# Performance work log

Hardware: AMD Instinct MI355X
Metric: run time of the kernel (lower is better)

## Reference

```python
import jax, jax.numpy as jnp
import numpy as np

B, N, M, D, NHEAD, FF, C, K = 2, 16384, 2048, 256, 8, 512, 50, 3
HID = 128          # embed/pos hidden
HEAD_HID = 256     # seg head hidden
L = 4              # depth
EPS = 1e-5


def setup_inputs() -> dict:
    key = jax.random.key(0)
    ks = jax.random.split(key, 32)
    g = lambda i, shape: jax.random.normal(ks[i], shape, dtype=jnp.float32) * 0.02
    z = lambda shape: jnp.zeros(shape, jnp.float32)
    o = lambda shape: jnp.ones(shape, jnp.float32)
    return {
        "xyz": jax.random.normal(ks[0], (B, N, 3), dtype=jnp.float32),
        "embed_w1": g(1, (3, HID)), "embed_b1": z((HID,)),
        "embed_w2": g(2, (HID, D)), "embed_b2": z((D,)),
        "pos_w1": g(3, (3, HID)), "pos_b1": z((HID,)),
        "pos_w2": g(4, (HID, D)), "pos_b2": z((D,)),
        "Wq": g(5, (L, D, D)), "bq": z((L, D)),
        "Wk": g(6, (L, D, D)), "bk": z((L, D)),
        "Wv": g(7, (L, D, D)), "bv": z((L, D)),
        "Wo": g(8, (L, D, D)), "bo": z((L, D)),
        "ln1_s": o((L, D)), "ln1_b": z((L, D)),
        "W1": g(9, (L, D, FF)), "b1": z((L, FF)),
        "W2": g(10, (L, FF, D)), "b2": z((L, D)),
        "ln2_s": o((L, D)), "ln2_b": z((L, D)),
        "head_w1": g(11, (D, HEAD_HID)), "head_b1": z((HEAD_HID,)),
        "head_w2": g(12, (HEAD_HID, C)), "head_b2": z((C,)),
    }


def _ln(x, s, b):
    m = x.mean(-1, keepdims=True)
    v = ((x - m) ** 2).mean(-1, keepdims=True)
    return (x - m) / jnp.sqrt(v + EPS) * s + b


def reference(xyz, embed_w1, embed_b1, embed_w2, embed_b2,
              pos_w1, pos_b1, pos_w2, pos_b2,
              Wq, bq, Wk, bk, Wv, bv, Wo, bo, ln1_s, ln1_b,
              W1, b1, W2, b2, ln2_s, ln2_b,
              head_w1, head_b1, head_w2, head_b2):
    # deterministic token subsample (replaces randperm stub): strided pick of M points
    stride = N // M
    tok = xyz[:, ::stride, :][:, :M]                                  # [B,M,3]
    # per-point embed + learned positional encoding
    x = jax.nn.relu(tok @ embed_w1 + embed_b1) @ embed_w2 + embed_b2  # [B,M,D]
    x = x + jax.nn.relu(tok @ pos_w1 + pos_b1) @ pos_w2 + pos_b2
    dh = D // NHEAD
    scale = 1.0 / jnp.sqrt(jnp.float32(dh))

    def layer(x, p):
        wq, bq_, wk, bk_, wv, bv_, wo, bo_, l1s, l1b, w1, b1_, w2, b2_, l2s, l2b = p
        # pre-norm MHSA
        y = _ln(x, l1s, l1b)
        q = (y @ wq + bq_).reshape(B, M, NHEAD, dh)
        k = (y @ wk + bk_).reshape(B, M, NHEAD, dh)
        v = (y @ wv + bv_).reshape(B, M, NHEAD, dh)
        att = jax.nn.softmax(jnp.einsum('bqhd,bkhd->bhqk', q, k) * scale, axis=-1)
        o = jnp.einsum('bhqk,bkhd->bqhd', att, v).reshape(B, M, D)
        x = x + o @ wo + bo_
        # pre-norm FFN (gelu, exact erf as in torch)
        y = _ln(x, l2s, l2b)
        x = x + jax.nn.gelu(y @ w1 + b1_, approximate=False) @ w2 + b2_
        return x, None

    x, _ = jax.lax.scan(layer, x, (Wq, bq, Wk, bk, Wv, bv, Wo, bo,
                                   ln1_s, ln1_b, W1, b1, W2, b2, ln2_s, ln2_b))
    logits_tok = jax.nn.relu(x @ head_w1 + head_b1) @ head_w2 + head_b2  # [B,M,C]

    # kNN propagation N->M: dist^2 = |q|^2 + |k|^2 - 2 q.k, topk smallest
    q2 = (xyz ** 2).sum(-1)[..., None]            # [B,N,1]
    k2 = (tok ** 2).sum(-1)[:, None, :]           # [B,1,M]
    dist = q2 + k2 - 2.0 * jnp.einsum('bnd,bmd->bnm', xyz, tok)
    dist = jax.lax.stop_gradient(jnp.maximum(dist, 0.0))
    idx = jax.lax.top_k(-dist, K)[1]              # [B,N,K]
    logits_nk = logits_tok[jnp.arange(B)[:, None, None], idx]  # [B,N,K,C]
    return logits_nk.mean(axis=2)                 # [B,N,C]
```

## Files before the change

kernel.cpp:

```cpp
#include <hip/hip_runtime.h>
#include <hip/hip_bf16.h>
#include <math.h>

#define B_ 2
#define N_ 16384
#define M_ 2048
#define D_ 256
#define NHEAD_ 8
#define DH_ 32
#define FF_ 512
#define C_ 50
#define HID_ 128
#define HHID_ 256
#define L_ 4
#define EPS_ 1e-5f
#define TOK_ (B_*M_)
#define QSCALE_ 0.25507604155757994f

typedef short short8 __attribute__((ext_vector_type(8)));
typedef short short4_t __attribute__((ext_vector_type(4)));
typedef float f32x4 __attribute__((ext_vector_type(4)));

__device__ __forceinline__ short f2bf(float f) {
  union { float f; unsigned u; } c; c.f = f;
  unsigned u = c.u;
  unsigned r = (u + 0x7FFFu + ((u >> 16) & 1u)) >> 16;
  return (short)r;
}
__device__ __forceinline__ float fast_exp2(float x) {
  float r;
  asm("v_exp_f32 %0, %1" : "=v"(r) : "v"(x));
  return r;
}
__device__ __forceinline__ unsigned cvt_pk_bf16(float lo, float hi) {
  unsigned r;
  asm("v_cvt_pk_bf16_f32 %0, %1, %2" : "=v"(r) : "v"(lo), "v"(hi));
  return r;
}

__device__ __forceinline__ void stage16(const short* __restrict__ g, short* lds,
                                        int rowStride, int tid) {
  int row = tid >> 2, gr = tid & 3;
  int kg = gr ^ (row & 3);
  __builtin_amdgcn_global_load_lds(
      (const __attribute__((address_space(1))) void*)(g + (size_t)row * rowStride + kg * 8),
      (__attribute__((address_space(3))) void*)(lds + tid * 8),
      16, 0, 0);
}

__global__ __launch_bounds__(256) void wconv_all(
    const float* __restrict__ Wq, const float* __restrict__ Wk,
    const float* __restrict__ Wv, const float* __restrict__ Wo,
    const float* __restrict__ W1, const float* __restrict__ W2,
    const float* __restrict__ h1,
    short* __restrict__ WqT, short* __restrict__ WkT,
    short* __restrict__ WvT, short* __restrict__ WoT,
    short* __restrict__ W1T, short* __restrict__ W2T, short* __restrict__ h1T) {
  int bid = blockIdx.x;
  const float* W; short* WT; int Kd, Nd, tn, tk;
  if (bid < 256) {
    int mat = bid >> 6, rem = bid & 63, l = rem >> 4, t = rem & 15;
    W  = (mat == 0 ? Wq : mat == 1 ? Wk : mat == 2 ? Wv : Wo) + l * 65536;
    WT = (mat == 0 ? WqT : mat == 1 ? WkT : mat == 2 ? WvT : WoT) + l * 65536;
    Kd = 256; Nd = 256; tn = t & 3; tk = t >> 2;
  } else if (bid < 384) {
    int rem = bid - 256, l = rem >> 5, t = rem & 31;
    W = W1 + l * 131072; WT = W1T + l * 131072;
    Kd = 256; Nd = 512; tn = t & 7; tk = t >> 3;
  } else if (bid < 512) {
    int rem = bid - 384, l = rem >> 5, t = rem & 31;
    W = W2 + l * 131072; WT = W2T + l * 131072;
    Kd = 512; Nd = 256; tn = t & 3; tk = t >> 2;
  } else {
    int t = bid - 512;
    W = h1; WT = h1T; Kd = 256; Nd = 256; tn = t & 3; tk = t >> 2;
  }
  int n0 = tn * 64, k0 = tk * 64;
  __shared__ short ts[64][72];
  int tid = threadIdx.x;
  #pragma unroll
  for (int i = 0; i < 4; ++i) {
    int r = i * 16 + (tid >> 4);
    int c4 = (tid & 15) * 4;
    float4 v = *(const float4*)&W[(size_t)(k0 + r) * Nd + n0 + c4];
    ts[c4 + 0][r] = f2bf(v.x);
    ts[c4 + 1][r] = f2bf(v.y);
    ts[c4 + 2][r] = f2bf(v.z);
    ts[c4 + 3][r] = f2bf(v.w);
  }
  __syncthreads();
  #pragma unroll
  for (int i = 0; i < 2; ++i) {
    int n = i * 32 + (tid >> 3);
    int kc = (tid & 7) * 8;
    *(short8*)&WT[(size_t)(n0 + n) * Kd + k0 + kc] = *(short8*)&ts[n][kc];
  }
}

__global__ __launch_bounds__(128) void embed_kernel(
    const float* __restrict__ xyz,
    const float* __restrict__ ew1, const float* __restrict__ eb1,
    const float* __restrict__ ew2, const float* __restrict__ eb2,
    const float* __restrict__ pw1, const float* __restrict__ pb1,
    const float* __restrict__ pw2, const float* __restrict__ pb2,
    float* __restrict__ x) {
  int t = blockIdx.x;
  int b = t / M_, m = t % M_;
  const float* p = xyz + ((size_t)b * N_ + (size_t)m * 8) * 3;
  float t0 = p[0], t1 = p[1], t2 = p[2];
  __shared__ float he[HID_], hp[HID_];
  int j = threadIdx.x;
  {
    float a = fmaf(t0, ew1[j], fmaf(t1, ew1[HID_ + j], fmaf(t2, ew1[2 * HID_ + j], eb1[j])));
    he[j] = fmaxf(a, 0.f);
    float c = fmaf(t0, pw1[j], fmaf(t1, pw1[HID_ + j], fmaf(t2, pw1[2 * HID_ + j], pb1[j])));
    hp[j] = fmaxf(c, 0.f);
  }
  __syncthreads();
  for (int d = j; d < D_; d += HID_) {
    float acc = eb2[d] + pb2[d];
    for (int k = 0; k < HID_; ++k) {
      acc = fmaf(he[k], ew2[k * D_ + d], acc);
      acc = fmaf(hp[k], pw2[k * D_ + d], acc);
    }
    x[(size_t)t * D_ + d] = acc;
  }
}

__global__ __launch_bounds__(256) void ln_fused(
    const float* __restrict__ x, const float* __restrict__ pa,
    const float* __restrict__ pb, const float* __restrict__ bias,
    const float* __restrict__ s, const float* __restrict__ bb,
    float* __restrict__ xw, short* __restrict__ y16) {
  int r = blockIdx.x * 4 + (threadIdx.x >> 6);
  int t = threadIdx.x & 63;
  float4 v = ((const float4*)(x + (size_t)r * D_))[t];
  if (pa) {
    float4 a = ((const float4*)(pa + (size_t)r * D_))[t];
    float4 c = ((const float4*)(pb + (size_t)r * D_))[t];
    float4 bi = ((const float4*)bias)[t];
    v.x += a.x + c.x + bi.x;
    v.y += a.y + c.y + bi.y;
    v.z += a.z + c.z + bi.z;
    v.w += a.w + c.w + bi.w;
    ((float4*)(xw + (size_t)r * D_))[t] = v;
  }
  float sum = v.x + v.y + v.z + v.w;
  #pragma unroll
  for (int o = 1; o < 64; o <<= 1) sum += __shfl_xor(sum, o, 64);
  float mean = sum * (1.f / D_);
  float dx = v.x - mean, dy = v.y - mean, dz = v.z - mean, dw = v.w - mean;
  float vs = dx * dx + dy * dy + dz * dz + dw * dw;
  #pragma unroll
  for (int o = 1; o < 64; o <<= 1) vs += __shfl_xor(vs, o, 64);
  float inv = 1.0f / sqrtf(vs * (1.f / D_) + EPS_);
  float4 sv = ((const float4*)s)[t];
  float4 bv = ((const float4*)bb)[t];
  short4_t ov;
  ov[0] = f2bf(dx * inv * sv.x + bv.x);
  ov[1] = f2bf(dy * inv * sv.y + bv.y);
  ov[2] = f2bf(dz * inv * sv.z + bv.z);
  ov[3] = f2bf(dw * inv * sv.w + bv.w);
  *(short4_t*)(y16 + (size_t)r * D_ + t * 4) = ov;
}

__global__ __launch_bounds__(256) void head2_kernel(
    const float* __restrict__ pa, const float* __restrict__ pb,
    const float* __restrict__ b1h, const float* __restrict__ w2,
    const float* __restrict__ b2, float* __restrict__ lt) {
  __shared__ float ys[4][HHID_];
  int w = threadIdx.x >> 6, l = threadIdx.x & 63;
  int t = blockIdx.x * 4 + w;
  float4 a = ((const float4*)(pa + (size_t)t * HHID_))[l];
  float4 c = ((const float4*)(pb + (size_t)t * HHID_))[l];
  float4 bi = ((const float4*)b1h)[l];
  float4 v;
  v.x = fmaxf(a.x + c.x + bi.x, 0.f);
  v.y = fmaxf(a.y + c.y + bi.y, 0.f);
  v.z = fmaxf(a.z + c.z + bi.z, 0.f);
  v.w = fmaxf(a.w + c.w + bi.w, 0.f);
  *(float4*)&ys[w][l * 4] = v;
  int cc = l < C_ ? l : 0;
  float a0 = 0.f, a1 = 0.f, a2 = 0.f, a3 = 0.f;
  #pragma unroll 4
  for (int k = 0; k < HHID_; k += 4) {
    a0 = fmaf(ys[w][k + 0], w2[(k + 0) * C_ + cc], a0);
    a1 = fmaf(ys[w][k + 1], w2[(k + 1) * C_ + cc], a1);
    a2 = fmaf(ys[w][k + 2], w2[(k + 2) * C_ + cc], a2);
    a3 = fmaf(ys[w][k + 3], w2[(k + 3) * C_ + cc], a3);
  }
  if (l < C_) lt[(size_t)t * C_ + l] = (a0 + a1) + (a2 + a3) + b2[l];
}

template <int ACT, int RES>
__device__ __forceinline__ void gemm16_body(
    const short* __restrict__ A16, const short* __restrict__ WT,
    const float* __restrict__ bias, const float* __restrict__ R,
    float* __restrict__ C, short* __restrict__ C16, short* __restrict__ VT,
    float oscale, int K, int Ncols, int m0, int n0) {
  __shared__ short As[64][32];
  __shared__ short Bs[64][32];
  int tid = threadIdx.x;
  int w = tid >> 6, l = tid & 63;
  int lq = l & 15, lg = l >> 4;
  int wr = (w & 1) * 32, wc = (w >> 1) * 32;
  int ga = (lg ^ (lq & 3)) * 8;
  f32x4 acc00 = {0.f, 0.f, 0.f, 0.f};
  f32x4 acc01 = {0.f, 0.f, 0.f, 0.f};
  f32x4 acc10 = {0.f, 0.f, 0.f, 0.f};
  f32x4 acc11 = {0.f, 0.f, 0.f, 0.f};
  for (int kk = 0; kk < K; kk += 32) {
    __syncthreads();
    stage16(A16 + (size_t)m0 * K + kk, &As[0][0], K, tid);
    stage16(WT + (size_t)n0 * K + kk, &Bs[0][0], K, tid);
    __syncthreads();
    short8 a0 = *(short8*)&As[wr + lq][ga];
    short8 a1 = *(short8*)&As[wr + 16 + lq][ga];
    short8 b0 = *(short8*)&Bs[wc + lq][ga];
    short8 b1 = *(short8*)&Bs[wc + 16 + lq][ga];
    acc00 = __builtin_amdgcn_mfma_f32_16x16x32_bf16(a0, b0, acc00, 0, 0, 0);
    acc01 = __builtin_amdgcn_mfma_f32_16x16x32_bf16(a0, b1, acc01, 0, 0, 0);
    acc10 = __builtin_amdgcn_mfma_f32_16x16x32_bf16(a1, b0, acc10, 0, 0, 0);
    acc11 = __builtin_amdgcn_mfma_f32_16x16x32_bf16(a1, b1, acc11, 0, 0, 0);
  }
  #pragma unroll
  for (int fi = 0; fi < 2; ++fi) {
    int row = m0 + wr + fi * 16 + lg * 4;
    #pragma unroll
    for (int fj = 0; fj < 2; ++fj) {
      int col = n0 + wc + fj * 16 + lq;
      short4_t vt4;
      #pragma unroll
      for (int r = 0; r < 4; ++r) {
        float v = (fi == 0 ? (fj == 0 ? acc00[r] : acc01[r])
                           : (fj == 0 ? acc10[r] : acc11[r])) + bias[col];
        if (ACT == 1) v = fmaxf(v, 0.f);
        else if (ACT == 2) v = 0.5f * v * (1.f + erff(v * 0.70710678118654752f));
        if (RES) v += R[(size_t)(row + r) * Ncols + col];
        if (C)   C[(size_t)(row + r) * Ncols + col] = v;
        if (C16) C16[(size_t)(row + r) * Ncols + col] = f2bf(v * oscale);
        if (VT)  vt4[r] = f2bf(v);
      }
      if (VT) {
        int bb = row >> 11, mm = row & (M_ - 1);
        *(short4_t*)&VT[((size_t)(bb * 256 + col)) * M_ + mm] = vt4;
      }
    }
  }
}

template <int ACT, int RES>
__global__ __launch_bounds__(256) void gemm16(
    const short* __restrict__ A16, const short* __restrict__ WT,
    const float* __restrict__ bias, const float* __restrict__ R,
    float* __restrict__ C, short* __restrict__ C16,
    int K, int Ncols) {
  gemm16_body<ACT, RES>(A16, WT, bias, R, C, C16, nullptr, 1.f, K, Ncols,
                        blockIdx.y * 64, blockIdx.x * 64);
}

__global__ __launch_bounds__(256) void gemm16_part(
    const short* __restrict__ A16, const short* __restrict__ WT,
    float* __restrict__ P, int K, int Klen, int Ncols) {
  __shared__ short As[64][32];
  __shared__ short Bs[64][32];
  int tid = threadIdx.x;
  int w = tid >> 6, l = tid & 63;
  int lq = l & 15, lg = l >> 4;
  int wr = (w & 1) * 32, wc = (w >> 1) * 32;
  int ga = (lg ^ (lq & 3)) * 8;
  int m0 = blockIdx.y * 64, n0 = blockIdx.x * 64;
  int k0 = blockIdx.z * Klen;
  f32x4 acc00 = {0.f, 0.f, 0.f, 0.f};
  f32x4 acc01 = {0.f, 0.f, 0.f, 0.f};
  f32x4 acc10 = {0.f, 0.f, 0.f, 0.f};
  f32x4 acc11 = {0.f, 0.f, 0.f, 0.f};
  for (int kk = k0; kk < k0 + Klen; kk += 32) {
    __syncthreads();
    stage16(A16 + (size_t)m0 * K + kk, &As[0][0], K, tid);
    stage16(WT + (size_t)n0 * K + kk, &Bs[0][0], K, tid);
    __syncthreads();
    short8 a0 = *(short8*)&As[wr + lq][ga];
    short8 a1 = *(short8*)&As[wr + 16 + lq][ga];
    short8 b0 = *(short8*)&Bs[wc + lq][ga];
    short8 b1 = *(short8*)&Bs[wc + 16 + lq][ga];
    acc00 = __builtin_amdgcn_mfma_f32_16x16x32_bf16(a0, b0, acc00, 0, 0, 0);
    acc01 = __builtin_amdgcn_mfma_f32_16x16x32_bf16(a0, b1, acc01, 0, 0, 0);
    acc10 = __builtin_amdgcn_mfma_f32_16x16x32_bf16(a1, b0, acc10, 0, 0, 0);
    acc11 = __builtin_amdgcn_mfma_f32_16x16x32_bf16(a1, b1, acc11, 0, 0, 0);
  }
  float* Pp = P + (size_t)blockIdx.z * TOK_ * Ncols;
  #pragma unroll
  for (int fi = 0; fi < 2; ++fi) {
    int row = m0 + wr + fi * 16 + lg * 4;
    #pragma unroll
    for (int fj = 0; fj < 2; ++fj) {
      int col = n0 + wc + fj * 16 + lq;
      #pragma unroll
      for (int r = 0; r < 4; ++r) {
        float v = (fi == 0 ? (fj == 0 ? acc00[r] : acc01[r])
                           : (fj == 0 ? acc10[r] : acc11[r]));
        Pp[(size_t)(row + r) * Ncols + col] = v;
      }
    }
  }
}

__global__ __launch_bounds__(256) void qkv16(
    const short* __restrict__ A16,
    const short* __restrict__ WqT, const short* __restrict__ WkT, const short* __restrict__ WvT,
    const float* __restrict__ bq, const float* __restrict__ bk, const float* __restrict__ bv,
    short* __restrict__ q16, short* __restrict__ k16, short* __restrict__ vt16) {
  int sel = blockIdx.x >> 2;
  int n0 = (blockIdx.x & 3) << 6;
  int m0 = blockIdx.y * 64;
  if (sel == 0) {
    gemm16_body<0, 0>(A16, WqT, bq, nullptr, nullptr, q16, nullptr, QSCALE_, D_, D_, m0, n0);
  } else if (sel == 1) {
    gemm16_body<0, 0>(A16, WkT, bk, nullptr, nullptr, k16, nullptr, 1.f, D_, D_, m0, n0);
  } else {
    gemm16_body<0, 0>(A16, WvT, bv, nullptr, nullptr, nullptr, vt16, 1.f, D_, D_, m0, n0);
  }
}

__global__ __launch_bounds__(256) void wo_split(
    const float* __restrict__ po0, const float* __restrict__ po1,
    const float* __restrict__ pl, const short* __restrict__ WT,
    float* __restrict__ P) {
  __shared__ short As[64][136];
  __shared__ short Bs[64][32];
  int tid = threadIdx.x;
  int w = tid >> 6, l = tid & 63;
  int m0 = blockIdx.y * 64, n0 = blockIdx.x * 64;
  int half = blockIdx.z;
  int c2 = l * 2;
  int hh = half * 4 + (c2 >> 5);
  int d0 = c2 & 31;
  #pragma unroll 4
  for (int c = 0; c < 16; ++c) {
    int t = w * 16 + c;
    int row = m0 + t;
    int bb = row >> 11, mm = row & (M_ - 1);
    size_t f = (size_t)(bb * NHEAD_ + hh) * M_ + mm;
    float inv = 1.f / (pl[f] + pl[16 * M_ + f]);
    float v0 = (po0[f * 32 + d0] + po1[f * 32 + d0]) * inv;
    float v1 = (po0[f * 32 + d0 + 1] + po1[f * 32 + d0 + 1]) * inv;
    *(unsigned*)&As[t][c2] = cvt_pk_bf16(v0, v1);
  }
  int lq = l & 15, lg = l >> 4;
  int wr = (w & 1) * 32, wc = (w >> 1) * 32;
  int gb = (lg ^ (lq & 3)) * 8;
  f32x4 acc00 = {0.f, 0.f, 0.f, 0.f};
  f32x4 acc01 = {0.f, 0.f, 0.f, 0.f};
  f32x4 acc10 = {0.f, 0.f, 0.f, 0.f};
  f32x4 acc11 = {0.f, 0.f, 0.f, 0.f};
  for (int kk = 0; kk < 128; kk += 32) {
    __syncthreads();
    stage16(WT + (size_t)n0 * D_ + half * 128 + kk, &Bs[0][0], D_, tid);
    __syncthreads();
    short8 a0 = *(short8*)&As[wr + lq][kk + lg * 8];
    short8 a1 = *(short8*)&As[wr + 16 + lq][kk + lg * 8];
    short8 b0 = *(short8*)&Bs[wc + lq][gb];
    short8 b1 = *(short8*)&Bs[wc + 16 + lq][gb];
    acc00 = __builtin_amdgcn_mfma_f32_16x16x32_bf16(a0, b0, acc00, 0, 0, 0);
    acc01 = __builtin_amdgcn_mfma_f32_16x16x32_bf16(a0, b1, acc01, 0, 0, 0);
    acc10 = __builtin_amdgcn_mfma_f32_16x16x32_bf16(a1, b0, acc10, 0, 0, 0);
    acc11 = __builtin_amdgcn_mfma_f32_16x16x32_bf16(a1, b1, acc11, 0, 0, 0);
  }
  float* Pp = P + (size_t)half * TOK_ * D_;
  #pragma unroll
  for (int fi = 0; fi < 2; ++fi) {
    int row = m0 + wr + fi * 16 + lg * 4;
    #pragma unroll
    for (int fj = 0; fj < 2; ++fj) {
      int col = n0 + wc + fj * 16 + lq;
      #pragma unroll
      for (int r = 0; r < 4; ++r) {
        float v = (fi == 0 ? (fj == 0 ? acc00[r] : acc01[r])
                           : (fj == 0 ? acc10[r] : acc11[r]));
        Pp[(size_t)(row + r) * D_ + col] = v;
      }
    }
  }
}

__global__ __launch_bounds__(256) void attn_mfma_kernel(
    const short* __restrict__ q16, const short* __restrict__ k16,
    const short* __restrict__ vt16,
    float* __restrict__ po0, float* __restrict__ po1,
    float* __restrict__ pl) {
  __shared__ short Ks[128][40];
  __shared__ short Vt[32][136];
  __shared__ short Ps[4][16][136];
  int bid = blockIdx.x;
  int half = bid & 1;
  int qt = (bid >> 1) & 31;
  int h  = (bid >> 6) & 7;
  int b  = bid >> 9;
  int tid = threadIdx.x;
  int w  = tid >> 6;
  int l  = tid & 63;
  int lq = l & 15;
  int lg = l >> 4;

  short8 qf = *(const short8*)&q16[(size_t)(b * M_ + qt * 64 + w * 16 + lq) * D_ + h * DH_ + lg * 8];

  const short one = (short)0x3F80;
  short8 ones = {one, one, one, one, one, one, one, one};

  f32x4 lacc = {0.f, 0.f, 0.f, 0.f};
  f32x4 o0 = {0.f, 0.f, 0.f, 0.f};
  f32x4 o1 = {0.f, 0.f, 0.f, 0.f};
  int srow = tid >> 1, scol = (tid & 1) * 16;
  int vd = tid >> 3, vm = (tid & 7) * 16;
  const short* kp = k16 + (size_t)(b * M_ + half * 1024 + srow) * D_ + h * DH_ + scol;
  const short* vp = vt16 + (size_t)((b * NHEAD_ + h) * DH_ + vd) * M_ + half * 1024 + vm;

  for (int kt = 0; kt < 8; ++kt) {
    __syncthreads();
    {
      const short* kg = kp + (size_t)(kt * 128) * D_;
      *(short8*)&Ks[srow][scol]     = *(const short8*)(kg);
      *(short8*)&Ks[srow][scol + 8] = *(const short8*)(kg + 8);
      const short* vg = vp + kt * 128;
      *(short8*)&Vt[vd][vm]     = *(const short8*)(vg);
      *(short8*)&Vt[vd][vm + 8] = *(const short8*)(vg + 8);
    }
    __syncthreads();
    f32x4 st[8];
    #pragma unroll
    for (int t = 0; t < 8; ++t) {
      short8 kf = *(short8*)&Ks[t * 16 + lq][lg * 8];
      f32x4 z = {0.f, 0.f, 0.f, 0.f};
      st[t] = __builtin_amdgcn_mfma_f32_16x16x32_bf16(kf, qf, z, 0, 0, 0);
    }
    #pragma unroll
    for (int t = 0; t < 8; ++t)
      #pragma unroll
      for (int r2 = 0; r2 < 4; ++r2)
        st[t][r2] = fast_exp2(st[t][r2]);
    {
      unsigned* pw = (unsigned*)&Ps[w][lq][0];
      #pragma unroll
      for (int t = 0; t < 8; ++t) {
        uint2 pk;
        pk.x = cvt_pk_bf16(st[t][0], st[t][1]);
        pk.y = cvt_pk_bf16(st[t][2], st[t][3]);
        *(uint2*)(pw + t * 8 + lg * 2) = pk;
      }
    }
    #pragma unroll
    for (int c = 0; c < 4; ++c) {
      short8 pf = *(short8*)&Ps[w][lq][c * 32 + lg * 8];
      short8 v0 = *(short8*)&Vt[lq][c * 32 + lg * 8];
      short8 v1 = *(short8*)&Vt[16 + lq][c * 32 + lg * 8];
      o0 = __builtin_amdgcn_mfma_f32_16x16x32_bf16(v0, pf, o0, 0, 0, 0);
      o1 = __builtin_amdgcn_mfma_f32_16x16x32_bf16(v1, pf, o1, 0, 0, 0);
      lacc = __builtin_amdgcn_mfma_f32_16x16x32_bf16(ones, pf, lacc, 0, 0, 0);
    }
  }
  int f = (b * NHEAD_ + h) * M_ + qt * 64 + w * 16 + lq;
  float* pp = (half == 0 ? po0 : po1) + (size_t)f * 32;
  #pragma unroll
  for (int r2 = 0; r2 < 4; ++r2) pp[lg * 4 + r2] = o0[r2];
  #pragma unroll
  for (int r2 = 0; r2 < 4; ++r2) pp[16 + lg * 4 + r2] = o1[r2];
  if (lg == 0) pl[half * (16 * M_) + f] = lacc[0];
}

__global__ __launch_bounds__(512) void knn_kernel(
    const float* __restrict__ xyz, const float* __restrict__ lt,
    float* __restrict__ out) {
  __shared__ float4 tok[2064];
  int b = blockIdx.x >> 9;
  int q0 = (blockIdx.x & 511) << 5;
  int tid = threadIdx.x;
  for (int i = tid; i < M_; i += 512) {
    const float* tp = xyz + ((size_t)b * N_ + (size_t)i * 8) * 3;
    float a = tp[0], bb = tp[1], cc = tp[2];
    tok[i + (i >> 7)] = make_float4(a, bb, cc, a * a + bb * bb + cc * cc);
  }
  __syncthreads();
  int g = tid >> 4, sl = tid & 15;
  int n = q0 + g;
  const float* qp = xyz + ((size_t)b * N_ + n) * 3;
  float qx = qp[0], qy = qp[1], qz = qp[2];
  float q2 = qx * qx + qy * qy + qz * qz;
  float dd0 = INFINITY, dd1 = INFINITY, dd2 = INFINITY;
  int ii0 = 0, ii1 = 0, ii2 = 0;
  const float4* cp = &tok[sl * 129];
  int mb = sl << 7;
  #pragma unroll 2
  for (int j = 0; j < 128; ++j) {
    float4 t = cp[j];
    float dot = fmaf(qx, t.x, fmaf(qy, t.y, qz * t.z));
    float d = fmaxf(q2 + t.w - 2.f * dot, 0.f);
    if (d < dd2) {
      int m = mb + j;
      if (d < dd1) {
        dd2 = dd1; ii2 = ii1;
        if (d < dd0) { dd1 = dd0; ii1 = ii0; dd0 = d; ii0 = m; }
        else         { dd1 = d;  ii1 = m; }
      } else         { dd2 = d;  ii2 = m; }
    }
  }
  auto insT = [&](float d, int i) {
    if (d < dd2 || (d == dd2 && i < ii2)) {
      if (d < dd1 || (d == dd1 && i < ii1)) {
        dd2 = dd1; ii2 = ii1;
        if (d < dd0 || (d == dd0 && i < ii0)) { dd1 = dd0; ii1 = ii0; dd0 = d; ii0 = i; }
        else { dd1 = d; ii1 = i; }
      } else { dd2 = d; ii2 = i; }
    }
  };
  #pragma unroll
  for (int off = 1; off < 16; off <<= 1) {
    float p0 = __shfl_xor(dd0, off, 64); int pi0 = __shfl_xor(ii0, off, 64);
    float p1 = __shfl_xor(dd1, off, 64); int pi1 = __shfl_xor(ii1, off, 64);
    float p2 = __shfl_xor(dd2, off, 64); int pi2 = __shfl_xor(ii2, off, 64);
    insT(p0, pi0); insT(p1, pi1); insT(p2, pi2);
  }
  const float* l0 = lt + ((size_t)b * M_ + ii0) * C_;
  const float* l1 = lt + ((size_t)b * M_ + ii1) * C_;
  const float* l2 = lt + ((size_t)b * M_ + ii2) * C_;
  float* op = out + ((size_t)b * N_ + n) * C_;
  for (int cc = sl; cc < C_; cc += 16)
    op[cc] = (l0[cc] + l1[cc] + l2[cc]) * (1.f / 3.f);
}

extern "C" void kernel_launch(void* const* d_in, const int* in_sizes, int n_in,
                              void* d_out, int out_size, void* d_ws, size_t ws_size,
                              hipStream_t stream) {
  const float* xyz  = (const float*)d_in[0];
  const float* ew1  = (const float*)d_in[1];
  const float* eb1  = (const float*)d_in[2];
  const float* ew2  = (const float*)d_in[3];
  const float* eb2  = (const float*)d_in[4];
  const float* pw1  = (const float*)d_in[5];
  const float* pb1  = (const float*)d_in[6];
  const float* pw2  = (const float*)d_in[7];
  const float* pb2  = (const float*)d_in[8];
  const float* Wq   = (const float*)d_in[9];
  const float* bq   = (const float*)d_in[10];
  const float* Wk   = (const float*)d_in[11];
  const float* bk   = (const float*)d_in[12];
  const float* Wv   = (const float*)d_in[13];
  const float* bv   = (const float*)d_in[14];
  const float* Wo   = (const float*)d_in[15];
  const float* bo   = (const float*)d_in[16];
  const float* ln1s = (const float*)d_in[17];
  const float* ln1b = (const float*)d_in[18];
  const float* W1   = (const float*)d_in[19];
  const float* b1   = (const float*)d_in[20];
  const float* W2   = (const float*)d_in[21];
  const float* b2   = (const float*)d_in[22];
  const float* ln2s = (const float*)d_in[23];
  const float* ln2b = (const float*)d_in[24];
  const float* hw1  = (const float*)d_in[25];
  const float* hb1  = (const float*)d_in[26];
  const float* hw2  = (const float*)d_in[27];
  const float* hb2  = (const float*)d_in[28];
  float* out = (float*)d_out;

  float* x   = (float*)d_ws;
  float* y   = x + 1048576;
  float* po2 = y + 1048576;
  float* po3 = po2 + 1048576;
  float* lt  = po3 + 1048576;
  short* y16 = (short*)(lt + 204800);
  short* q16 = y16 + 1048576;
  short* k16 = q16 + 1048576;
  short* v16 = k16 + 1048576;
  short* vt16 = v16 + 1048576;
  short* ob16 = vt16 + 1048576;
  short* x16  = ob16 + 1048576;
  short* ff16 = x16 + 1048576;
  short* WqT = ff16 + 2097152;
  short* WkT = WqT + 262144;
  short* WvT = WkT + 262144;
  short* WoT = WvT + 262144;
  short* W1T = WoT + 262144;
  short* W2T = W1T + 524288;
  short* h1T = W2T + 524288;
  float* wpart = (float*)(h1T + 65536);
  float* po0 = y;
  float* po1 = (float*)ff16;
  float* pl  = lt;

  wconv_all<<<528, 256, 0, stream>>>(Wq, Wk, Wv, Wo, W1, W2, hw1,
                                     WqT, WkT, WvT, WoT, W1T, W2T, h1T);
  embed_kernel<<<TOK_, 128, 0, stream>>>(xyz, ew1, eb1, ew2, eb2, pw1, pb1, pw2, pb2, x);

  dim3 gQKV(12, TOK_ / 64);
  dim3 gDs(D_ / 64, TOK_ / 64, 2);
  dim3 gF(FF_ / 64, TOK_ / 64);
  dim3 gD(D_ / 64, TOK_ / 64);
  for (int l = 0; l < L_; ++l) {
    if (l == 0)
      ln_fused<<<TOK_ / 4, 256, 0, stream>>>(x, nullptr, nullptr, nullptr,
                                             ln1s + l * D_, ln1b + l * D_, x, y16);
    else
      ln_fused<<<TOK_ / 4, 256, 0, stream>>>(x, wpart, wpart + (size_t)TOK_ * D_,
                                             b2 + (l - 1) * D_,
                                             ln1s + l * D_, ln1b + l * D_, x, y16);
    qkv16<<<gQKV, 256, 0, stream>>>(y16, WqT + l * 65536, WkT + l * 65536, WvT + l * 65536,
                                    bq + l * D_, bk + l * D_, bv + l * D_, q16, k16, vt16);
    attn_mfma_kernel<<<1024, 256, 0, stream>>>(q16, k16, vt16, po0, po1, pl);
    wo_split<<<gDs, 256, 0, stream>>>(po0, po1, pl, WoT + l * 65536, wpart);
    ln_fused<<<TOK_ / 4, 256, 0, stream>>>(x, wpart, wpart + (size_t)TOK_ * D_,
                                           bo + l * D_,
                                           ln2s + l * D_, ln2b + l * D_, x, y16);
    gemm16<2, 0><<<gF, 256, 0, stream>>>(y16, W1T + l * 131072, b1 + l * FF_, nullptr, nullptr, ff16, D_, FF_);
    if (l < L_ - 1) {
      gemm16_part<<<gDs, 256, 0, stream>>>(ff16, W2T + l * 131072, wpart, FF_, 256, D_);
    } else {
      gemm16<0, 1><<<gD, 256, 0, stream>>>(ff16, W2T + l * 131072, b2 + l * D_, x, x, x16, FF_, D_);
    }
  }
  gemm16_part<<<gDs, 256, 0, stream>>>(x16, h1T, wpart, D_, 128, HHID_);
  head2_kernel<<<TOK_ / 4, 256, 0, stream>>>(wpart, wpart + (size_t)TOK_ * HHID_,
                                             hb1, hw2, hb2, lt);
  knn_kernel<<<1024, 512, 0, stream>>>(xyz, lt, out);
}
```

Baseline: 376.2 us.

## Prefetch next K/V tile into registers and halve attention P scratch buffer

The attention kernel now loads the next K and V tile from global memory into registers while the current tile is being computed, so global latency overlaps the MFMA and exp work. The probability scratch tile Ps is cut to half its width and filled in two halves, each consumed by its PV MFMAs before the next half is written, which reduces shared-memory use per block and may allow more resident blocks. In exchange it uses more registers for the prefetched data, which could lower occupancy, and adds more ordering between LDS writes and reads within each wave.

```diff
diff --git a/kernel.cpp b/kernel.cpp
--- a/kernel.cpp
+++ b/kernel.cpp
@@ -391,7 +391,7 @@
     float* __restrict__ pl) {
   __shared__ short Ks[128][40];
   __shared__ short Vt[32][136];
-  __shared__ short Ps[4][16][136];
+  __shared__ short Ps[4][16][72];
   int bid = blockIdx.x;
   int half = bid & 1;
   int qt = (bid >> 1) & 31;
@@ -416,15 +416,25 @@
   const short* kp = k16 + (size_t)(b * M_ + half * 1024 + srow) * D_ + h * DH_ + scol;
   const short* vp = vt16 + (size_t)((b * NHEAD_ + h) * DH_ + vd) * M_ + half * 1024 + vm;
 
+  short8 ka0 = *(const short8*)(kp);
+  short8 ka1 = *(const short8*)(kp + 8);
+  short8 va0 = *(const short8*)(vp);
+  short8 va1 = *(const short8*)(vp + 8);
+
   for (int kt = 0; kt < 8; ++kt) {
     __syncthreads();
-    {
-      const short* kg = kp + (size_t)(kt * 128) * D_;
-      *(short8*)&Ks[srow][scol]     = *(const short8*)(kg);
-      *(short8*)&Ks[srow][scol + 8] = *(const short8*)(kg + 8);
-      const short* vg = vp + kt * 128;
-      *(short8*)&Vt[vd][vm]     = *(const short8*)(vg);
-      *(short8*)&Vt[vd][vm + 8] = *(const short8*)(vg + 8);
+    *(short8*)&Ks[srow][scol]     = ka0;
+    *(short8*)&Ks[srow][scol + 8] = ka1;
+    *(short8*)&Vt[vd][vm]         = va0;
+    *(short8*)&Vt[vd][vm + 8]     = va1;
+    short8 nk0, nk1, nv0, nv1;
+    if (kt < 7) {
+      const short* kg = kp + (size_t)((kt + 1) * 128) * D_;
+      nk0 = *(const short8*)(kg);
+      nk1 = *(const short8*)(kg + 8);
+      const short* vg = vp + (kt + 1) * 128;
+      nv0 = *(const short8*)(vg);
+      nv1 = *(const short8*)(vg + 8);
     }
     __syncthreads();
     f32x4 st[8];
@@ -439,18 +449,16 @@
       #pragma unroll
       for (int r2 = 0; r2 < 4; ++r2)
         st[t][r2] = fast_exp2(st[t][r2]);
-    {
-      unsigned* pw = (unsigned*)&Ps[w][lq][0];
-      #pragma unroll
-      for (int t = 0; t < 8; ++t) {
-        uint2 pk;
-        pk.x = cvt_pk_bf16(st[t][0], st[t][1]);
-        pk.y = cvt_pk_bf16(st[t][2], st[t][3]);
-        *(uint2*)(pw + t * 8 + lg * 2) = pk;
-      }
-    }
-    #pragma unroll
-    for (int c = 0; c < 4; ++c) {
+    unsigned* pw = (unsigned*)&Ps[w][lq][0];
+    #pragma unroll
+    for (int t = 0; t < 4; ++t) {
+      uint2 pk;
+      pk.x = cvt_pk_bf16(st[t][0], st[t][1]);
+      pk.y = cvt_pk_bf16(st[t][2], st[t][3]);
+      *(uint2*)(pw + t * 8 + lg * 2) = pk;
+    }
+    #pragma unroll
+    for (int c = 0; c < 2; ++c) {
       short8 pf = *(short8*)&Ps[w][lq][c * 32 + lg * 8];
       short8 v0 = *(short8*)&Vt[lq][c * 32 + lg * 8];
       short8 v1 = *(short8*)&Vt[16 + lq][c * 32 + lg * 8];
@@ -458,6 +466,23 @@
       o1 = __builtin_amdgcn_mfma_f32_16x16x32_bf16(v1, pf, o1, 0, 0, 0);
       lacc = __builtin_amdgcn_mfma_f32_16x16x32_bf16(ones, pf, lacc, 0, 0, 0);
     }
+    #pragma unroll
+    for (int t = 4; t < 8; ++t) {
+      uint2 pk;
+      pk.x = cvt_pk_bf16(st[t][0], st[t][1]);
+      pk.y = cvt_pk_bf16(st[t][2], st[t][3]);
+      *(uint2*)(pw + (t - 4) * 8 + lg * 2) = pk;
+    }
+    #pragma unroll
+    for (int c = 2; c < 4; ++c) {
+      short8 pf = *(short8*)&Ps[w][lq][(c - 2) * 32 + lg * 8];
+      short8 v0 = *(short8*)&Vt[lq][c * 32 + lg * 8];
+      short8 v1 = *(short8*)&Vt[16 + lq][c * 32 + lg * 8];
+      o0 = __builtin_amdgcn_mfma_f32_16x16x32_bf16(v0, pf, o0, 0, 0, 0);
+      o1 = __builtin_amdgcn_mfma_f32_16x16x32_bf16(v1, pf, o1, 0, 0, 0);
+      lacc = __builtin_amdgcn_mfma_f32_16x16x32_bf16(ones, pf, lacc, 0, 0, 0);
+    }
+    ka0 = nk0; ka1 = nk1; va0 = nv0; va1 = nv1;
   }
   int f = (b * NHEAD_ + h) * M_ + qt * 64 + w * 16 + lq;
   float* pp = (half == 0 ? po0 : po1) + (size_t)f * 32;
```

Result: faster. 366.8 us, median of 2 (-2.5%).
